# Optimization experiments

Hardware: AMD Instinct MI355X
Metric: run time of the kernel (lower is better)

The kernel has to match this reference:

```python
import jax, jax.numpy as jnp
import numpy as np
import math

EPS = 1e-6  # PCEN eps


def _logit(p):
    return math.log(p / (1.0 - p))


def _pcen(mel, log_s, log_alpha, log_delta, log_r, dmin, dmax):
    """PCEN: per-channel energy normalization. mel: (B, M, T); params: (M,)."""
    s = jnp.clip(jax.nn.sigmoid(log_s), 0.05, 0.3)            # (M,)
    alpha = jnp.clip(jax.nn.sigmoid(log_alpha), 0.9, 0.999)   # (M,)
    delta = jnp.clip(jnp.exp(log_delta), dmin, dmax)          # (M,)
    r = jnp.clip(jax.nn.sigmoid(log_r), 0.05, 0.25)           # (M,)

    # IIR smoother over time: smoother_0 = mel[..., 0];
    # for t in 0..T-1: smoother = (1-s)*smoother + s*mel_t  (t=0 included -> smoothed_0 = mel_0)
    mel_t = jnp.transpose(mel, (2, 0, 1))  # (T, B, M)

    def step(sm, x):
        sm = (1.0 - s) * sm + s * x
        return sm, sm

    _, smoothed_t = jax.lax.scan(step, mel_t[0], mel_t)
    smoothed = jnp.transpose(smoothed_t, (1, 2, 0))  # (B, M, T)

    gain = (EPS + smoothed) ** (-alpha[None, :, None])
    d = delta[None, :, None]
    rr = r[None, :, None]
    return (mel * gain + d) ** rr - d ** rr


def setup_inputs() -> dict:
    key = jax.random.key(0)
    B, M, T = 64, 80, 4000
    mel = jax.random.uniform(key, (B, M, T), dtype=jnp.float32)
    f = jnp.full
    return {
        "mel": mel,
        # non-stationary expert PCEN (s=0.025, alpha=0.99, delta=2.0, r=0.5)
        "log_s_ns": f((M,), _logit(0.025), jnp.float32),
        "log_alpha_ns": f((M,), _logit(0.99), jnp.float32),
        "log_delta_ns": f((M,), math.log(2.0), jnp.float32),
        "log_r_ns": f((M,), _logit(0.5), jnp.float32),
        # stationary expert PCEN (s=0.15, alpha=0.99, delta=0.01, r=0.1)
        "log_s_st": f((M,), _logit(0.15), jnp.float32),
        "log_alpha_st": f((M,), _logit(0.99), jnp.float32),
        "log_delta_st": f((M,), math.log(0.01), jnp.float32),
        "log_r_st": f((M,), _logit(0.1), jnp.float32),
        "gate_temp": jnp.asarray(5.0, jnp.float32),
    }


def reference(mel, log_s_ns, log_alpha_ns, log_delta_ns, log_r_ns,
              log_s_st, log_alpha_st, log_delta_st, log_r_st, gate_temp):
    out_ns = _pcen(mel, log_s_ns, log_alpha_ns, log_delta_ns, log_r_ns, 0.5, 5.0)
    out_st = _pcen(mel, log_s_st, log_alpha_st, log_delta_st, log_r_st, 0.001, 0.1)

    # routing signal: spectral flatness + spectral tilt (0 learnable params)
    log_mel = jnp.log(mel + 1e-8)
    geo = jnp.exp(jnp.mean(log_mel, axis=1, keepdims=True))          # (B,1,T)
    arith = jnp.mean(mel, axis=1, keepdims=True) + 1e-8
    sf = jnp.clip(geo / arith, 0.0, 1.0)

    M = mel.shape[1]
    low = jnp.mean(mel[:, : M // 3, :], axis=1, keepdims=True)
    high = jnp.mean(mel[:, 2 * M // 3 :, :], axis=1, keepdims=True)
    tilt = jnp.clip(low / (low + high + 1e-8), 0.0, 1.0)

    sf_adj = sf + (1.0 - sf) * jax.nn.relu(tilt - 0.6)
    gate = jax.nn.sigmoid(gate_temp * (sf_adj - 0.5))
    return gate * out_st + (1.0 - gate) * out_ns
```

## Files before the change

kernel.cpp:

```cpp
#include <hip/hip_runtime.h>
#include <math.h>

static constexpr int kM = 80;
static constexpr int kT = 4000;
static constexpr int kB = 64;
static constexpr int kLow = kM / 3;
static constexpr int kHighStart = 2 * kM / 3;
static constexpr int kHighCount = kM - kHighStart;
#define EPSF 1e-6f
#define LOG2E 1.4426950408889634f

typedef float vfloat4 __attribute__((ext_vector_type(4)));
typedef float vfloat2 __attribute__((ext_vector_type(2)));

__device__ __forceinline__ float hw_exp2(float x) { return __builtin_amdgcn_exp2f(x); }
__device__ __forceinline__ float hw_log2(float x) { return __builtin_amdgcn_logf(x); }

__device__ __forceinline__ float fast_sigmoid(float x) {
    return __builtin_amdgcn_rcpf(1.0f + hw_exp2(-x * LOG2E));
}

__global__ __launch_bounds__(256) void gate_kernel(
    const float* __restrict__ mel,
    const float* __restrict__ gate_temp,
    float* __restrict__ gate)
{
    const int lane = threadIdx.x & 63;
    const int wid  = threadIdx.x >> 6;
    const int b    = blockIdx.y;
    const int t0   = blockIdx.x * 256 + lane * 4;
    const bool valid = (t0 < kT);

    const float* base = mel + (size_t)b * kM * kT + t0;

    vfloat4 slog = {0.f,0.f,0.f,0.f}, ssum = {0.f,0.f,0.f,0.f};
    vfloat4 slow = {0.f,0.f,0.f,0.f}, shigh = {0.f,0.f,0.f,0.f};

    const int m0 = wid * 20;
    if (valid) {
        #pragma unroll
        for (int j = 0; j < 20; ++j) {
            const int m = m0 + j;
            const vfloat4 v = *reinterpret_cast<const vfloat4*>(base + (size_t)m * kT);
            vfloat4 lg;
            lg.x = hw_log2(v.x + 1e-8f); lg.y = hw_log2(v.y + 1e-8f);
            lg.z = hw_log2(v.z + 1e-8f); lg.w = hw_log2(v.w + 1e-8f);
            slog += lg;
            ssum += v;
            if (m < kLow)        slow  += v;
            if (m >= kHighStart) shigh += v;
        }
    }

    __shared__ vfloat4 sh[4][4][64];
    sh[wid][0][lane] = slog;
    sh[wid][1][lane] = ssum;
    sh[wid][2][lane] = slow;
    sh[wid][3][lane] = shigh;
    __syncthreads();

    if (wid == 0 && valid) {
        slog  = sh[0][0][lane] + sh[1][0][lane] + sh[2][0][lane] + sh[3][0][lane];
        ssum  = sh[0][1][lane] + sh[1][1][lane] + sh[2][1][lane] + sh[3][1][lane];
        slow  = sh[0][2][lane] + sh[1][2][lane] + sh[2][2][lane] + sh[3][2][lane];
        shigh = sh[0][3][lane] + sh[1][3][lane] + sh[2][3][lane] + sh[3][3][lane];

        const float gt = gate_temp[0];
        float sl[4]  = {slog.x, slog.y, slog.z, slog.w};
        float ss[4]  = {ssum.x, ssum.y, ssum.z, ssum.w};
        float lo[4]  = {slow.x, slow.y, slow.z, slow.w};
        float hi[4]  = {shigh.x, shigh.y, shigh.z, shigh.w};
        float g4[4];
        #pragma unroll
        for (int q = 0; q < 4; ++q) {
            const float geo   = hw_exp2(sl[q] * (1.0f / kM));
            const float arith = ss[q] * (1.0f / kM) + 1e-8f;
            float sf = geo * __builtin_amdgcn_rcpf(arith);
            sf = fminf(fmaxf(sf, 0.0f), 1.0f);
            const float low  = lo[q] * (1.0f / kLow);
            const float high = hi[q] * (1.0f / kHighCount);
            float tilt = low * __builtin_amdgcn_rcpf(low + high + 1e-8f);
            tilt = fminf(fmaxf(tilt, 0.0f), 1.0f);
            const float sfa = sf + (1.0f - sf) * fmaxf(tilt - 0.6f, 0.0f);
            g4[q] = fast_sigmoid(gt * (sfa - 0.5f));
        }
        vfloat4 o; o.x = g4[0]; o.y = g4[1]; o.z = g4[2]; o.w = g4[3];
        *reinterpret_cast<vfloat4*>(gate + (size_t)b * kT + t0) = o;
    }
}

__global__ __launch_bounds__(256, 8) void pcen_kernel(
    const float* __restrict__ mel,
    const float* __restrict__ ls_ns, const float* __restrict__ la_ns,
    const float* __restrict__ ld_ns, const float* __restrict__ lr_ns,
    const float* __restrict__ ls_st, const float* __restrict__ la_st,
    const float* __restrict__ ld_st, const float* __restrict__ lr_st,
    const float* __restrict__ gate,
    float* __restrict__ out)
{
    const int m = blockIdx.x;
    const int b = blockIdx.y;

    const float s_ns     = fminf(fmaxf(fast_sigmoid(ls_ns[m]), 0.05f), 0.3f);
    const float alpha_ns = fminf(fmaxf(fast_sigmoid(la_ns[m]), 0.9f), 0.999f);
    const float delta_ns = fminf(fmaxf(hw_exp2(ld_ns[m] * LOG2E), 0.5f), 5.0f);
    const float r_ns     = fminf(fmaxf(fast_sigmoid(lr_ns[m]), 0.05f), 0.25f);
    const float s_st     = fminf(fmaxf(fast_sigmoid(ls_st[m]), 0.05f), 0.3f);
    const float alpha_st = fminf(fmaxf(fast_sigmoid(la_st[m]), 0.9f), 0.999f);
    const float delta_st = fminf(fmaxf(hw_exp2(ld_st[m] * LOG2E), 0.001f), 0.1f);
    const float r_st     = fminf(fmaxf(fast_sigmoid(lr_st[m]), 0.05f), 0.25f);
    const float dr_ns = hw_exp2(r_ns * hw_log2(delta_ns));
    const float dr_st = hw_exp2(r_st * hw_log2(delta_st));

    const vfloat2 a2 = {1.0f - s_ns, 1.0f - s_st};
    const vfloat2 s2 = {s_ns, s_st};
    const vfloat2 d2 = {delta_ns, delta_st};
    const float man = -alpha_ns, mas = -alpha_st;

    const size_t rowoff = ((size_t)b * kM + m) * kT;
    const float* row = mel + rowoff;

    const int tid = threadIdx.x;
    const int t0  = tid * 16;
    const bool valid = (t0 < kT);

    float x[16];
    float gv[16];
    if (valid) {
        const float4* p = reinterpret_cast<const float4*>(row + t0);
        #pragma unroll
        for (int q = 0; q < 4; ++q) {
            const float4 v = p[q];
            x[4*q+0] = v.x; x[4*q+1] = v.y; x[4*q+2] = v.z; x[4*q+3] = v.w;
        }
        const float4* gp = reinterpret_cast<const float4*>(gate + (size_t)b * kT + t0);
        #pragma unroll
        for (int q = 0; q < 4; ++q) {
            const float4 v = gp[q];
            gv[4*q+0] = v.x; gv[4*q+1] = v.y; gv[4*q+2] = v.z; gv[4*q+3] = v.w;
        }
    } else {
        #pragma unroll
        for (int k = 0; k < 16; ++k) { x[k] = 0.0f; gv[k] = 0.0f; }
    }

    __shared__ float sv0;
    if (tid == 0) sv0 = x[0];

    vfloat2 Av = {1.0f, 1.0f}, Bv = {0.0f, 0.0f};
    if (valid) {
        #pragma unroll
        for (int k = 0; k < 16; ++k) {
            Bv = a2 * Bv + s2 * x[k];
        }
        const vfloat2 p2 = a2 * a2;
        const vfloat2 p4 = p2 * p2;
        const vfloat2 p8 = p4 * p4;
        Av = p8 * p8;
    }

    const int lane = tid & 63;
    const int wid  = tid >> 6;

    #pragma unroll
    for (int d = 1; d < 64; d <<= 1) {
        const float qAn = __shfl_up(Av.x, d);
        const float qAs = __shfl_up(Av.y, d);
        const float qBn = __shfl_up(Bv.x, d);
        const float qBs = __shfl_up(Bv.y, d);
        if (lane >= d) {
            const vfloat2 qA = {qAn, qAs};
            const vfloat2 qB = {qBn, qBs};
            Bv = Av * qB + Bv;
            Av = Av * qA;
        }
    }

    __shared__ vfloat2 wA[4], wB[4];
    if (lane == 63) { wA[wid] = Av; wB[wid] = Bv; }
    __syncthreads();

    vfloat2 eA, eB;
    eA.x = __shfl_up(Av.x, 1); eA.y = __shfl_up(Av.y, 1);
    eB.x = __shfl_up(Bv.x, 1); eB.y = __shfl_up(Bv.y, 1);
    if (lane == 0) { eA = (vfloat2){1.0f, 1.0f}; eB = (vfloat2){0.0f, 0.0f}; }

    vfloat2 pA = {1.0f, 1.0f}, pB = {0.0f, 0.0f};
    for (int j = 0; j < wid; ++j) {
        pB = wA[j] * pB + wB[j];
        pA = wA[j] * pA;
    }

    const vfloat2 v0 = {sv0, sv0};
    vfloat2 sm = eA * (pA * v0 + pB) + eB;

    if (valid) {
        float res[16];
        #pragma unroll
        for (int k = 0; k < 16; ++k) {
            const float xv = x[k];
            sm = a2 * sm + s2 * xv;
            vfloat2 g2;
            g2.x = hw_exp2(man * hw_log2(sm.x + EPSF));
            g2.y = hw_exp2(mas * hw_log2(sm.y + EPSF));
            const vfloat2 u2 = g2 * xv + d2;
            const float on = hw_exp2(r_ns * hw_log2(u2.x)) - dr_ns;
            const float os = hw_exp2(r_st * hw_log2(u2.y)) - dr_st;
            res[k] = fmaf(gv[k], os - on, on);
        }

        float4* op = reinterpret_cast<float4*>(out + rowoff + t0);
        #pragma unroll
        for (int q = 0; q < 4; ++q) {
            float4 v;
            v.x = res[4*q+0]; v.y = res[4*q+1]; v.z = res[4*q+2]; v.w = res[4*q+3];
            op[q] = v;
        }
    }
}

extern "C" void kernel_launch(void* const* d_in, const int* in_sizes, int n_in,
                              void* d_out, int out_size, void* d_ws, size_t ws_size,
                              hipStream_t stream)
{
    const float* mel       = (const float*)d_in[0];
    const float* ls_ns     = (const float*)d_in[1];
    const float* la_ns     = (const float*)d_in[2];
    const float* ld_ns     = (const float*)d_in[3];
    const float* lr_ns     = (const float*)d_in[4];
    const float* ls_st     = (const float*)d_in[5];
    const float* la_st     = (const float*)d_in[6];
    const float* ld_st     = (const float*)d_in[7];
    const float* lr_st     = (const float*)d_in[8];
    const float* gate_temp = (const float*)d_in[9];
    float* out  = (float*)d_out;
    float* gate = (float*)d_ws;

    dim3 gA(16, kB);
    gate_kernel<<<gA, 256, 0, stream>>>(mel, gate_temp, gate);

    dim3 gB(kM, kB);
    pcen_kernel<<<gB, 256, 0, stream>>>(mel, ls_ns, la_ns, ld_ns, lr_ns,
                                        ls_st, la_st, ld_st, lr_st, gate, out);
}
```

Baseline: 183.7 us.

## Fuse gate and PCEN into one chunked kernel with warm-up scan windows

Merges the gate kernel and the PCEN kernel into one launch. Each block takes a 512-column time chunk of one batch item, computes the gate into shared memory, and computes the per-channel parameters once into shared memory. Each wave then runs the IIR scan over 10 channels, using a 256-sample warm-up window before its chunk in place of a true cross-chunk carry. This drops the gate round-trip through global memory and a kernel launch. In exchange the scan does about 1.5x extra work, the grid is much smaller, and the result becomes approximate: the warm-up relies on the clamped s >= 0.05 making the start-of-window state error decay to negligible size.

```diff
diff --git a/kernel.cpp b/kernel.cpp
--- a/kernel.cpp
+++ b/kernel.cpp
@@ -7,6 +7,10 @@
 static constexpr int kLow = kM / 3;
 static constexpr int kHighStart = 2 * kM / 3;
 static constexpr int kHighCount = kM - kHighStart;
+static constexpr int kC = 512;
+static constexpr int kW = 256;
+static constexpr int kE = 12;
+static constexpr int kChunks = 8;
 #define EPSF 1e-6f
 #define LOG2E 1.4426950408889634f
 
@@ -20,201 +24,153 @@
     return __builtin_amdgcn_rcpf(1.0f + hw_exp2(-x * LOG2E));
 }
 
-__global__ __launch_bounds__(256) void gate_kernel(
-    const float* __restrict__ mel,
-    const float* __restrict__ gate_temp,
-    float* __restrict__ gate)
-{
-    const int lane = threadIdx.x & 63;
-    const int wid  = threadIdx.x >> 6;
-    const int b    = blockIdx.y;
-    const int t0   = blockIdx.x * 256 + lane * 4;
-    const bool valid = (t0 < kT);
-
-    const float* base = mel + (size_t)b * kM * kT + t0;
-
-    vfloat4 slog = {0.f,0.f,0.f,0.f}, ssum = {0.f,0.f,0.f,0.f};
-    vfloat4 slow = {0.f,0.f,0.f,0.f}, shigh = {0.f,0.f,0.f,0.f};
-
-    const int m0 = wid * 20;
-    if (valid) {
-        #pragma unroll
-        for (int j = 0; j < 20; ++j) {
-            const int m = m0 + j;
-            const vfloat4 v = *reinterpret_cast<const vfloat4*>(base + (size_t)m * kT);
-            vfloat4 lg;
-            lg.x = hw_log2(v.x + 1e-8f); lg.y = hw_log2(v.y + 1e-8f);
-            lg.z = hw_log2(v.z + 1e-8f); lg.w = hw_log2(v.w + 1e-8f);
-            slog += lg;
-            ssum += v;
-            if (m < kLow)        slow  += v;
-            if (m >= kHighStart) shigh += v;
-        }
-    }
-
-    __shared__ vfloat4 sh[4][4][64];
-    sh[wid][0][lane] = slog;
-    sh[wid][1][lane] = ssum;
-    sh[wid][2][lane] = slow;
-    sh[wid][3][lane] = shigh;
-    __syncthreads();
-
-    if (wid == 0 && valid) {
-        slog  = sh[0][0][lane] + sh[1][0][lane] + sh[2][0][lane] + sh[3][0][lane];
-        ssum  = sh[0][1][lane] + sh[1][1][lane] + sh[2][1][lane] + sh[3][1][lane];
-        slow  = sh[0][2][lane] + sh[1][2][lane] + sh[2][2][lane] + sh[3][2][lane];
-        shigh = sh[0][3][lane] + sh[1][3][lane] + sh[2][3][lane] + sh[3][3][lane];
-
-        const float gt = gate_temp[0];
-        float sl[4]  = {slog.x, slog.y, slog.z, slog.w};
-        float ss[4]  = {ssum.x, ssum.y, ssum.z, ssum.w};
-        float lo[4]  = {slow.x, slow.y, slow.z, slow.w};
-        float hi[4]  = {shigh.x, shigh.y, shigh.z, shigh.w};
-        float g4[4];
-        #pragma unroll
-        for (int q = 0; q < 4; ++q) {
-            const float geo   = hw_exp2(sl[q] * (1.0f / kM));
-            const float arith = ss[q] * (1.0f / kM) + 1e-8f;
-            float sf = geo * __builtin_amdgcn_rcpf(arith);
-            sf = fminf(fmaxf(sf, 0.0f), 1.0f);
-            const float low  = lo[q] * (1.0f / kLow);
-            const float high = hi[q] * (1.0f / kHighCount);
-            float tilt = low * __builtin_amdgcn_rcpf(low + high + 1e-8f);
-            tilt = fminf(fmaxf(tilt, 0.0f), 1.0f);
-            const float sfa = sf + (1.0f - sf) * fmaxf(tilt - 0.6f, 0.0f);
-            g4[q] = fast_sigmoid(gt * (sfa - 0.5f));
-        }
-        vfloat4 o; o.x = g4[0]; o.y = g4[1]; o.z = g4[2]; o.w = g4[3];
-        *reinterpret_cast<vfloat4*>(gate + (size_t)b * kT + t0) = o;
-    }
-}
-
-__global__ __launch_bounds__(256, 8) void pcen_kernel(
+__global__ __launch_bounds__(512) void fused_kernel(
     const float* __restrict__ mel,
     const float* __restrict__ ls_ns, const float* __restrict__ la_ns,
     const float* __restrict__ ld_ns, const float* __restrict__ lr_ns,
     const float* __restrict__ ls_st, const float* __restrict__ la_st,
     const float* __restrict__ ld_st, const float* __restrict__ lr_st,
-    const float* __restrict__ gate,
+    const float* __restrict__ gate_temp,
     float* __restrict__ out)
 {
-    const int m = blockIdx.x;
-    const int b = blockIdx.y;
+    const int j   = blockIdx.x;
+    const int b   = blockIdx.y;
+    const int c0  = j * kC;
+    const int tid = threadIdx.x;
+    const int lane = tid & 63;
+    const int wid  = tid >> 6;
 
-    const float s_ns     = fminf(fmaxf(fast_sigmoid(ls_ns[m]), 0.05f), 0.3f);
-    const float alpha_ns = fminf(fmaxf(fast_sigmoid(la_ns[m]), 0.9f), 0.999f);
-    const float delta_ns = fminf(fmaxf(hw_exp2(ld_ns[m] * LOG2E), 0.5f), 5.0f);
-    const float r_ns     = fminf(fmaxf(fast_sigmoid(lr_ns[m]), 0.05f), 0.25f);
-    const float s_st     = fminf(fmaxf(fast_sigmoid(ls_st[m]), 0.05f), 0.3f);
-    const float alpha_st = fminf(fmaxf(fast_sigmoid(la_st[m]), 0.9f), 0.999f);
-    const float delta_st = fminf(fmaxf(hw_exp2(ld_st[m] * LOG2E), 0.001f), 0.1f);
-    const float r_st     = fminf(fmaxf(fast_sigmoid(lr_st[m]), 0.05f), 0.25f);
-    const float dr_ns = hw_exp2(r_ns * hw_log2(delta_ns));
-    const float dr_st = hw_exp2(r_st * hw_log2(delta_st));
+    __shared__ float gate_s[kC];
+    __shared__ vfloat4 prm[kM][3];
 
-    const vfloat2 a2 = {1.0f - s_ns, 1.0f - s_st};
-    const vfloat2 s2 = {s_ns, s_st};
-    const vfloat2 d2 = {delta_ns, delta_st};
-    const float man = -alpha_ns, mas = -alpha_st;
-
-    const size_t rowoff = ((size_t)b * kM + m) * kT;
-    const float* row = mel + rowoff;
-
-    const int tid = threadIdx.x;
-    const int t0  = tid * 16;
-    const bool valid = (t0 < kT);
-
-    float x[16];
-    float gv[16];
-    if (valid) {
-        const float4* p = reinterpret_cast<const float4*>(row + t0);
-        #pragma unroll
-        for (int q = 0; q < 4; ++q) {
-            const float4 v = p[q];
-            x[4*q+0] = v.x; x[4*q+1] = v.y; x[4*q+2] = v.z; x[4*q+3] = v.w;
-        }
-        const float4* gp = reinterpret_cast<const float4*>(gate + (size_t)b * kT + t0);
-        #pragma unroll
-        for (int q = 0; q < 4; ++q) {
-            const float4 v = gp[q];
-            gv[4*q+0] = v.x; gv[4*q+1] = v.y; gv[4*q+2] = v.z; gv[4*q+3] = v.w;
-        }
-    } else {
-        #pragma unroll
-        for (int k = 0; k < 16; ++k) { x[k] = 0.0f; gv[k] = 0.0f; }
+    if (tid < kM) {
+        const int m = tid;
+        const float s_ns     = fminf(fmaxf(fast_sigmoid(ls_ns[m]), 0.05f), 0.3f);
+        const float alpha_ns = fminf(fmaxf(fast_sigmoid(la_ns[m]), 0.9f), 0.999f);
+        const float delta_ns = fminf(fmaxf(hw_exp2(ld_ns[m] * LOG2E), 0.5f), 5.0f);
+        const float r_ns     = fminf(fmaxf(fast_sigmoid(lr_ns[m]), 0.05f), 0.25f);
+        const float s_st     = fminf(fmaxf(fast_sigmoid(ls_st[m]), 0.05f), 0.3f);
+        const float alpha_st = fminf(fmaxf(fast_sigmoid(la_st[m]), 0.9f), 0.999f);
+        const float delta_st = fminf(fmaxf(hw_exp2(ld_st[m] * LOG2E), 0.001f), 0.1f);
+        const float r_st     = fminf(fmaxf(fast_sigmoid(lr_st[m]), 0.05f), 0.25f);
+        vfloat4 w0; w0.x = 1.0f - s_ns; w0.y = 1.0f - s_st; w0.z = s_ns; w0.w = s_st;
+        vfloat4 w1; w1.x = delta_ns; w1.y = delta_st; w1.z = -alpha_ns; w1.w = -alpha_st;
+        vfloat4 w2; w2.x = r_ns; w2.y = r_st;
+        w2.z = hw_exp2(r_ns * hw_log2(delta_ns));
+        w2.w = hw_exp2(r_st * hw_log2(delta_st));
+        prm[m][0] = w0; prm[m][1] = w1; prm[m][2] = w2;
     }
 
-    __shared__ float sv0;
-    if (tid == 0) sv0 = x[0];
+    {
+        const int col = c0 + tid;
+        if (col < kT) {
+            const float* base = mel + (size_t)b * kM * kT + col;
+            float slog = 0.f, ssum = 0.f, slow = 0.f, shigh = 0.f;
+            #pragma unroll
+            for (int m = 0; m < kM; ++m) {
+                const float v = base[(size_t)m * kT];
+                slog += hw_log2(v + 1e-8f);
+                ssum += v;
+                if (m < kLow)        slow  += v;
+                if (m >= kHighStart) shigh += v;
+            }
+            const float geo   = hw_exp2(slog * (1.0f / kM));
+            const float arith = ssum * (1.0f / kM) + 1e-8f;
+            float sf = geo * __builtin_amdgcn_rcpf(arith);
+            sf = fminf(fmaxf(sf, 0.0f), 1.0f);
+            const float low  = slow  * (1.0f / kLow);
+            const float high = shigh * (1.0f / kHighCount);
+            float tilt = low * __builtin_amdgcn_rcpf(low + high + 1e-8f);
+            tilt = fminf(fmaxf(tilt, 0.0f), 1.0f);
+            const float sfa = sf + (1.0f - sf) * fmaxf(tilt - 0.6f, 0.0f);
+            gate_s[tid] = fast_sigmoid(gate_temp[0] * (sfa - 0.5f));
+        }
+    }
+    __syncthreads();
 
-    vfloat2 Av = {1.0f, 1.0f}, Bv = {0.0f, 0.0f};
-    if (valid) {
+    const int ws = (j == 0) ? 0 : (c0 - kW);
+    const int base_col = ws + lane * kE;
+    const bool xvalid = (base_col + kE <= kT);
+
+    for (int i = 0; i < 10; ++i) {
+        const int m = wid * 10 + i;
+        const vfloat4 w0 = prm[m][0];
+        const vfloat4 w1 = prm[m][1];
+        const vfloat4 w2 = prm[m][2];
+        const vfloat2 a2 = {w0.x, w0.y};
+        const vfloat2 s2 = {w0.z, w0.w};
+        const vfloat2 d2 = {w1.x, w1.y};
+        const float man = w1.z, mas = w1.w;
+        const float r_ns = w2.x, r_st = w2.y, dr_ns = w2.z, dr_st = w2.w;
+        const size_t rowoff = (size_t)(b * kM + m) * kT;
+
+        float x[kE];
+        if (xvalid) {
+            const vfloat4* rp = reinterpret_cast<const vfloat4*>(mel + rowoff + base_col);
+            #pragma unroll
+            for (int q = 0; q < 3; ++q) {
+                const vfloat4 v = rp[q];
+                x[4*q+0] = v.x; x[4*q+1] = v.y; x[4*q+2] = v.z; x[4*q+3] = v.w;
+            }
+        } else {
+            #pragma unroll
+            for (int k = 0; k < kE; ++k) x[k] = 0.0f;
+        }
+
+        vfloat2 Bv = {0.0f, 0.0f};
         #pragma unroll
-        for (int k = 0; k < 16; ++k) {
-            Bv = a2 * Bv + s2 * x[k];
-        }
+        for (int k = 0; k < kE; ++k) Bv = a2 * Bv + s2 * x[k];
         const vfloat2 p2 = a2 * a2;
         const vfloat2 p4 = p2 * p2;
         const vfloat2 p8 = p4 * p4;
-        Av = p8 * p8;
-    }
+        vfloat2 Av = p8 * p4;
 
-    const int lane = tid & 63;
-    const int wid  = tid >> 6;
-
-    #pragma unroll
-    for (int d = 1; d < 64; d <<= 1) {
-        const float qAn = __shfl_up(Av.x, d);
-        const float qAs = __shfl_up(Av.y, d);
-        const float qBn = __shfl_up(Bv.x, d);
-        const float qBs = __shfl_up(Bv.y, d);
-        if (lane >= d) {
-            const vfloat2 qA = {qAn, qAs};
-            const vfloat2 qB = {qBn, qBs};
-            Bv = Av * qB + Bv;
-            Av = Av * qA;
-        }
-    }
-
-    __shared__ vfloat2 wA[4], wB[4];
-    if (lane == 63) { wA[wid] = Av; wB[wid] = Bv; }
-    __syncthreads();
-
-    vfloat2 eA, eB;
-    eA.x = __shfl_up(Av.x, 1); eA.y = __shfl_up(Av.y, 1);
-    eB.x = __shfl_up(Bv.x, 1); eB.y = __shfl_up(Bv.y, 1);
-    if (lane == 0) { eA = (vfloat2){1.0f, 1.0f}; eB = (vfloat2){0.0f, 0.0f}; }
-
-    vfloat2 pA = {1.0f, 1.0f}, pB = {0.0f, 0.0f};
-    for (int j = 0; j < wid; ++j) {
-        pB = wA[j] * pB + wB[j];
-        pA = wA[j] * pA;
-    }
-
-    const vfloat2 v0 = {sv0, sv0};
-    vfloat2 sm = eA * (pA * v0 + pB) + eB;
-
-    if (valid) {
-        float res[16];
         #pragma unroll
-        for (int k = 0; k < 16; ++k) {
-            const float xv = x[k];
-            sm = a2 * sm + s2 * xv;
-            vfloat2 g2;
-            g2.x = hw_exp2(man * hw_log2(sm.x + EPSF));
-            g2.y = hw_exp2(mas * hw_log2(sm.y + EPSF));
-            const vfloat2 u2 = g2 * xv + d2;
-            const float on = hw_exp2(r_ns * hw_log2(u2.x)) - dr_ns;
-            const float os = hw_exp2(r_st * hw_log2(u2.y)) - dr_st;
-            res[k] = fmaf(gv[k], os - on, on);
+        for (int d = 1; d < 64; d <<= 1) {
+            const float qAn = __shfl_up(Av.x, d);
+            const float qAs = __shfl_up(Av.y, d);
+            const float qBn = __shfl_up(Bv.x, d);
+            const float qBs = __shfl_up(Bv.y, d);
+            if (lane >= d) {
+                const vfloat2 qA = {qAn, qAs};
+                const vfloat2 qB = {qBn, qBs};
+                Bv = Av * qB + Bv;
+                Av = Av * qA;
+            }
         }
 
-        float4* op = reinterpret_cast<float4*>(out + rowoff + t0);
+        vfloat2 eA, eB;
+        eA.x = __shfl_up(Av.x, 1); eA.y = __shfl_up(Av.y, 1);
+        eB.x = __shfl_up(Bv.x, 1); eB.y = __shfl_up(Bv.y, 1);
+        if (lane == 0) { eA = (vfloat2){1.0f, 1.0f}; eB = (vfloat2){0.0f, 0.0f}; }
+        const float x0 = __shfl(x[0], 0);
+        const vfloat2 v0 = {x0, x0};
+        vfloat2 sm = eA * v0 + eB;
+
         #pragma unroll
-        for (int q = 0; q < 4; ++q) {
-            float4 v;
-            v.x = res[4*q+0]; v.y = res[4*q+1]; v.z = res[4*q+2]; v.w = res[4*q+3];
-            op[q] = v;
+        for (int q = 0; q < 3; ++q) {
+            const int colq = base_col + 4 * q;
+            const bool emit = (colq >= c0) && (colq < c0 + kC) && (colq < kT);
+            vfloat4 g4 = {0.f, 0.f, 0.f, 0.f};
+            if (emit) g4 = *reinterpret_cast<const vfloat4*>(gate_s + (colq - c0));
+            vfloat4 r4;
+            #pragma unroll
+            for (int kk = 0; kk < 4; ++kk) {
+                const float xv = x[4*q+kk];
+                sm = a2 * sm + s2 * xv;
+                if (emit) {
+                    vfloat2 g2;
+                    g2.x = hw_exp2(man * hw_log2(sm.x + EPSF));
+                    g2.y = hw_exp2(mas * hw_log2(sm.y + EPSF));
+                    const vfloat2 u2 = g2 * xv + d2;
+                    const float on = hw_exp2(r_ns * hw_log2(u2.x)) - dr_ns;
+                    const float os = hw_exp2(r_st * hw_log2(u2.y)) - dr_st;
+                    r4[kk] = fmaf(g4[kk], os - on, on);
+                }
+            }
+            if (emit) {
+                *reinterpret_cast<vfloat4*>(out + rowoff + colq) = r4;
+            }
         }
     }
 }
@@ -234,12 +190,9 @@
     const float* lr_st     = (const float*)d_in[8];
     const float* gate_temp = (const float*)d_in[9];
     float* out  = (float*)d_out;
-    float* gate = (float*)d_ws;
 
-    dim3 gA(16, kB);
-    gate_kernel<<<gA, 256, 0, stream>>>(mel, gate_temp, gate);
-
-    dim3 gB(kM, kB);
-    pcen_kernel<<<gB, 256, 0, stream>>>(mel, ls_ns, la_ns, ld_ns, lr_ns,
-                                        ls_st, la_st, ld_st, lr_st, gate, out);
+    dim3 g(kChunks, kB);
+    fused_kernel<<<g, 512, 0, stream>>>(mel, ls_ns, la_ns, ld_ns, lr_ns,
+                                        ls_st, la_st, ld_st, lr_st,
+                                        gate_temp, out);
 }
```

After: 187.2 us. About the same (+1.9%).
